# Kernel tuning notes

Measured on AMD Instinct MI355X. Metric: run time of the kernel, lower is better.

## Reference

```python
import jax, jax.numpy as jnp
import numpy as np
import math

B, S, D, H = 2, 2048, 1024, 16
HD = D // H  # 64


def _rope(x, cos, sin):
    # x: [B,S,H,HD]; cos/sin: [S, HD//2]
    x2 = x.reshape(*x.shape[:-1], HD // 2, 2)
    x0, x1 = x2[..., 0], x2[..., 1]
    c = cos[None, :, None, :]
    s = sin[None, :, None, :]
    r0 = x0 * c - x1 * s
    r1 = x0 * s + x1 * c
    return jnp.stack([r0, r1], axis=-1).reshape(x.shape)


def setup_inputs() -> dict:
    key = jax.random.key(0)
    ks = jax.random.split(key, 6)
    x = jax.random.normal(ks[0], (B, S, D), dtype=jnp.float32)
    wq = jax.random.normal(ks[1], (D, D), dtype=jnp.float32) * 0.02
    wk = jax.random.normal(ks[2], (D, D), dtype=jnp.float32) * 0.02
    wv = jax.random.normal(ks[3], (D, D), dtype=jnp.float32) * 0.02
    wo = jax.random.normal(ks[4], (D, D), dtype=jnp.float32) * 0.02
    # standard RoPE frequencies: theta = 10000^(-2i/HD)
    inv_freq = 1.0 / (10000.0 ** (jnp.arange(0, HD, 2, dtype=jnp.float32) / HD))
    t = jnp.arange(S, dtype=jnp.float32)
    ang = t[:, None] * inv_freq[None, :]  # [S, HD//2]
    freqs_cos = jnp.cos(ang)
    freqs_sin = jnp.sin(ang)
    # causal additive mask [S, S]
    mask = jnp.where(jnp.tril(jnp.ones((S, S), dtype=bool)), 0.0, -1e9).astype(jnp.float32)
    return {"x": x, "wq": wq, "wk": wk, "wv": wv, "wo": wo,
            "freqs_cos": freqs_cos, "freqs_sin": freqs_sin, "mask": mask}


def reference(x, wq, wk, wv, wo, freqs_cos, freqs_sin, mask):
    b, s, d = x.shape
    # nn.Linear with no bias: y = x @ W^T
    q = jnp.einsum('bsd,od->bso', x, wq).reshape(b, s, H, HD)
    k = jnp.einsum('bsd,od->bso', x, wk).reshape(b, s, H, HD)
    v = jnp.einsum('bsd,od->bso', x, wv).reshape(b, s, H, HD)
    q = _rope(q, freqs_cos, freqs_sin)
    k = _rope(k, freqs_cos, freqs_sin)
    # [B,H,S,HD]
    q = q.transpose(0, 2, 1, 3)
    k = k.transpose(0, 2, 1, 3)
    v = v.transpose(0, 2, 1, 3)
    scores = jnp.einsum('bhqd,bhkd->bhqk', q, k) / math.sqrt(HD)
    scores = scores + mask[None, None, :, :]
    p = jax.nn.softmax(scores.astype(jnp.float32), axis=-1).astype(q.dtype)
    out = jnp.einsum('bhqk,bhkd->bhqd', p, v)
    out = out.transpose(0, 2, 1, 3).reshape(b, s, d)
    return jnp.einsum('bsd,od->bso', out, wo)
```

## Files before the change

### kernel.cpp

```cpp
#include <hip/hip_runtime.h>
#include <hip/hip_bf16.h>
#include <stdint.h>

#define NB 2
#define NS 2048
#define ND 1024
#define NH 16
#define NM (NB*NS)

typedef __attribute__((ext_vector_type(8))) short bf16x8;
typedef __attribute__((ext_vector_type(4))) float f32x4;

static __device__ __forceinline__ f32x4 mfma16(bf16x8 a, bf16x8 b, f32x4 c) {
  return __builtin_amdgcn_mfma_f32_16x16x32_bf16(a, b, c, 0, 0, 0);
}

static __device__ __forceinline__ void gload_lds16(const void* g, void* l) {
  __builtin_amdgcn_global_load_lds(
      (const __attribute__((address_space(1))) void*)g,
      (__attribute__((address_space(3))) void*)l, 16, 0, 0);
}

static __device__ __forceinline__ uint32_t pkbf2(float a, float b) {
  return (uint32_t)__bfloat16_as_ushort(__float2bfloat16(a)) |
         ((uint32_t)__bfloat16_as_ushort(__float2bfloat16(b)) << 16);
}

#define QSCALE 0.18033688011112042f

struct alignas(8) bh4 { __hip_bfloat16 x, y, z, w; };

__global__ void cvt_bf16(const float* __restrict__ in,
                         __hip_bfloat16* __restrict__ out, int n4) {
  int i = blockIdx.x * blockDim.x + threadIdx.x;
  int stride = gridDim.x * blockDim.x;
  for (; i < n4; i += stride) {
    float4 v = reinterpret_cast<const float4*>(in)[i];
    bh4 o;
    o.x = __float2bfloat16(v.x);
    o.y = __float2bfloat16(v.y);
    o.z = __float2bfloat16(v.z);
    o.w = __float2bfloat16(v.w);
    reinterpret_cast<bh4*>(out)[i] = o;
  }
}

__global__ void cvt_w4(const float* __restrict__ w0, const float* __restrict__ w1,
                       const float* __restrict__ w2, const float* __restrict__ w3,
                       __hip_bfloat16* o0, __hip_bfloat16* o1,
                       __hip_bfloat16* o2, __hip_bfloat16* o3) {
  const int t = blockIdx.x >> 10;
  const float* in = (t == 0) ? w0 : (t == 1) ? w1 : (t == 2) ? w2 : w3;
  __hip_bfloat16* out = (t == 0) ? o0 : (t == 1) ? o1 : (t == 2) ? o2 : o3;
  const int i = (blockIdx.x & 1023) * 256 + threadIdx.x;
  float4 v = reinterpret_cast<const float4*>(in)[i];
  bh4 o;
  o.x = __float2bfloat16(v.x);
  o.y = __float2bfloat16(v.y);
  o.z = __float2bfloat16(v.z);
  o.w = __float2bfloat16(v.w);
  reinterpret_cast<bh4*>(out)[i] = o;
}

__global__ __launch_bounds__(256) void gemm_qkv(
    const __hip_bfloat16* __restrict__ A,
    const __hip_bfloat16* __restrict__ Wq,
    const __hip_bfloat16* __restrict__ Wk,
    const __hip_bfloat16* __restrict__ Wv,
    const float* __restrict__ fcos,
    const float* __restrict__ fsin,
    __hip_bfloat16* __restrict__ Qo,
    __hip_bfloat16* __restrict__ Ko,
    __hip_bfloat16* __restrict__ Vo) {
  __shared__ __hip_bfloat16 sA[128 * 32];
  __shared__ __hip_bfloat16 sB[128 * 32];

  const int wsel = blockIdx.y >> 3;
  const __hip_bfloat16* W = (wsel == 0) ? Wq : (wsel == 1) ? Wk : Wv;

  const int tid = threadIdx.x;
  const int wid = tid >> 6;
  const int lane = tid & 63;
  const int l4 = lane >> 4, l16 = lane & 15;
  const int brow = blockIdx.x * 128;
  const int bcol = (blockIdx.y & 7) * 128;
  const int wr = (wid >> 1) * 64;
  const int wc = (wid & 1) * 64;

  f32x4 acc[4][4] = {};

  const __hip_bfloat16* Ap = A + (size_t)(brow + (tid >> 2)) * 1024 + (tid & 3) * 8;
  const __hip_bfloat16* Wp = W + (size_t)(bcol + (tid >> 2)) * 1024 + (tid & 3) * 8;
  char* sAc = (char*)sA + wid * 1024;
  char* sBc = (char*)sB + wid * 1024;

  for (int kt = 0; kt < 32; ++kt) {
    const int k0 = kt * 32;
    __syncthreads();
    gload_lds16(Ap + k0,             sAc);
    gload_lds16(Ap + 64 * 1024 + k0, sAc + 4096);
    gload_lds16(Wp + k0,             sBc);
    gload_lds16(Wp + 64 * 1024 + k0, sBc + 4096);
    __syncthreads();

    bf16x8 af[4], bfr[4];
#pragma unroll
    for (int i = 0; i < 4; ++i)
      af[i] = *(const bf16x8*)&sA[(wr + i * 16 + l16) * 32 + l4 * 8];
#pragma unroll
    for (int i = 0; i < 4; ++i)
      bfr[i] = *(const bf16x8*)&sB[(wc + i * 16 + l16) * 32 + l4 * 8];
#pragma unroll
    for (int mi = 0; mi < 4; ++mi)
#pragma unroll
      for (int ni = 0; ni < 4; ++ni)
        acc[mi][ni] = mfma16(af[mi], bfr[ni], acc[mi][ni]);
  }

#pragma unroll
  for (int mi = 0; mi < 4; ++mi)
#pragma unroll
    for (int ni = 0; ni < 4; ++ni)
#pragma unroll
      for (int j = 0; j < 4; ++j) {
        float v = acc[mi][ni][j];
        const int row = brow + wr + mi * 16 + l4 * 4 + j;
        const int col = bcol + wc + ni * 16 + l16;
        const int bb = row >> 11, ss = row & 2047;
        const int hh = col >> 6, hd = col & 63;
        if (wsel == 2) {
          Vo[((size_t)(bb * 16 + hh) * 64 + hd) * 2048 + ss] = __float2bfloat16(v);
        } else {
          float other = __shfl_xor(v, 1);
          const int p = hd >> 1;
          const float c = fcos[ss * 32 + p];
          const float sn = fsin[ss * 32 + p];
          float r = (col & 1) ? (other * sn + v * c) : (v * c - other * sn);
          __hip_bfloat16* dst = (wsel == 0) ? Qo : Ko;
          if (wsel == 0) r *= QSCALE;
          dst[((size_t)(bb * 16 + hh) * 2048 + ss) * 64 + hd] = __float2bfloat16(r);
        }
      }
}

__global__ __launch_bounds__(256) void gemm_out(
    const __hip_bfloat16* __restrict__ A,
    const __hip_bfloat16* __restrict__ W,
    float* __restrict__ C) {
  __shared__ __hip_bfloat16 sA[64 * 32];
  __shared__ __hip_bfloat16 sB[128 * 32];

  const int tid = threadIdx.x;
  const int wid = tid >> 6;
  const int lane = tid & 63;
  const int l4 = lane >> 4, l16 = lane & 15;
  const int brow = blockIdx.x * 64;
  const int bcol = blockIdx.y * 128;
  const int wr = (wid & 1) * 32;
  const int wc = (wid >> 1) * 64;

  f32x4 acc[2][4] = {};

  const __hip_bfloat16* Ap = A + (size_t)(brow + (tid >> 2)) * 1024 + (tid & 3) * 8;
  const __hip_bfloat16* Wp = W + (size_t)(bcol + (tid >> 2)) * 1024 + (tid & 3) * 8;
  char* sAc = (char*)sA + wid * 1024;
  char* sBc = (char*)sB + wid * 1024;

  for (int kt = 0; kt < 32; ++kt) {
    const int k0 = kt * 32;
    __syncthreads();
    gload_lds16(Ap + k0,             sAc);
    gload_lds16(Wp + k0,             sBc);
    gload_lds16(Wp + 64 * 1024 + k0, sBc + 4096);
    __syncthreads();

    bf16x8 af[2], bfr[4];
#pragma unroll
    for (int i = 0; i < 2; ++i)
      af[i] = *(const bf16x8*)&sA[(wr + i * 16 + l16) * 32 + l4 * 8];
#pragma unroll
    for (int i = 0; i < 4; ++i)
      bfr[i] = *(const bf16x8*)&sB[(wc + i * 16 + l16) * 32 + l4 * 8];
#pragma unroll
    for (int mi = 0; mi < 2; ++mi)
#pragma unroll
      for (int ni = 0; ni < 4; ++ni)
        acc[mi][ni] = mfma16(af[mi], bfr[ni], acc[mi][ni]);
  }

#pragma unroll
  for (int mi = 0; mi < 2; ++mi)
#pragma unroll
    for (int ni = 0; ni < 4; ++ni)
#pragma unroll
      for (int j = 0; j < 4; ++j) {
        const int row = brow + wr + mi * 16 + l4 * 4 + j;
        const int col = bcol + wc + ni * 16 + l16;
        C[(size_t)row * 1024 + col] = acc[mi][ni][j];
      }
}

__global__ __launch_bounds__(64) void attn_fwd(
    const __hip_bfloat16* __restrict__ Q,
    const __hip_bfloat16* __restrict__ K,
    const __hip_bfloat16* __restrict__ VT,
    __hip_bfloat16* __restrict__ AO) {
  const int L = blockIdx.x;
  const int g = 63 - (L >> 5);
  const int bh = L & 31;
  const int bb = bh >> 4;
  const int hh = bh & 15;
  const int lane = threadIdx.x & 63;
  const int l4 = lane >> 4, l16 = lane & 15;
  const int wq0 = g * 32;

  const __hip_bfloat16* Qg = Q + (size_t)bh * 2048 * 64;
  const __hip_bfloat16* Kg = K + (size_t)bh * 2048 * 64;
  const __hip_bfloat16* Vg = VT + (size_t)bh * 64 * 2048;

  __shared__ __hip_bfloat16 sP[32][72];

  bf16x8 qf[2][2];
#pragma unroll
  for (int q2 = 0; q2 < 2; ++q2)
#pragma unroll
    for (int dk = 0; dk < 2; ++dk)
      qf[q2][dk] = *(const bf16x8*)&Qg[(size_t)(wq0 + q2 * 16 + l16) * 64 + dk * 32 + l4 * 8];

  float mrun[2] = {-1e30f, -1e30f};
  float lrun[2] = {0.f, 0.f};
  f32x4 oacc[2][4] = {};

  const int lastkv = (wq0 + 31) >> 6;
  for (int kv = 0; kv <= lastkv; ++kv) {
    const int kb = kv * 64;

    bf16x8 kfr[4][2];
#pragma unroll
    for (int kf = 0; kf < 4; ++kf)
#pragma unroll
      for (int dk = 0; dk < 2; ++dk)
        kfr[kf][dk] = *(const bf16x8*)&Kg[(size_t)(kb + kf * 16 + l16) * 64 + dk * 32 + l4 * 8];

    f32x4 sacc[4][2] = {};
    __builtin_amdgcn_s_setprio(1);
#pragma unroll
    for (int dk = 0; dk < 2; ++dk)
#pragma unroll
      for (int kf = 0; kf < 4; ++kf)
#pragma unroll
        for (int q2 = 0; q2 < 2; ++q2)
          sacc[kf][q2] = mfma16(kfr[kf][dk], qf[q2][dk], sacc[kf][q2]);
    __builtin_amdgcn_s_setprio(0);

    bf16x8 vfr[4][2];
#pragma unroll
    for (int df = 0; df < 4; ++df)
#pragma unroll
      for (int ks = 0; ks < 2; ++ks)
        vfr[df][ks] = *(const bf16x8*)&Vg[(size_t)(df * 16 + l16) * 2048 + kb + ks * 32 + l4 * 8];

    const bool need_mask = (kb + 63 > wq0);
    float fac[2];
#pragma unroll
    for (int q2 = 0; q2 < 2; ++q2) {
      const int qi = wq0 + q2 * 16 + l16;
      float pv[16];
#pragma unroll
      for (int kf = 0; kf < 4; ++kf)
#pragma unroll
        for (int j = 0; j < 4; ++j) {
          float s = sacc[kf][q2][j];
          if (need_mask && (kb + kf * 16 + l4 * 4 + j > qi)) s = -1e30f;
          pv[kf * 4 + j] = s;
        }
      float m0 = fmaxf(fmaxf(pv[0], pv[1]), fmaxf(pv[2], pv[3]));
      float m1 = fmaxf(fmaxf(pv[4], pv[5]), fmaxf(pv[6], pv[7]));
      float m2 = fmaxf(fmaxf(pv[8], pv[9]), fmaxf(pv[10], pv[11]));
      float m3 = fmaxf(fmaxf(pv[12], pv[13]), fmaxf(pv[14], pv[15]));
      float mloc = fmaxf(fmaxf(m0, m1), fmaxf(m2, m3));
      mloc = fmaxf(mloc, __shfl_xor(mloc, 16));
      mloc = fmaxf(mloc, __shfl_xor(mloc, 32));
      const float mold = mrun[q2];
      const float mnew = fmaxf(mold, mloc);
      const float f = exp2f(mold - mnew);
      fac[q2] = f;
      mrun[q2] = mnew;
      float ts = 0.f;
      float pe[16];
#pragma unroll
      for (int t = 0; t < 16; ++t) { pe[t] = exp2f(pv[t] - mnew); ts += pe[t]; }
#pragma unroll
      for (int kf = 0; kf < 4; ++kf) {
        uint2 w;
        w.x = pkbf2(pe[kf * 4 + 0], pe[kf * 4 + 1]);
        w.y = pkbf2(pe[kf * 4 + 2], pe[kf * 4 + 3]);
        *(uint2*)&sP[q2 * 16 + l16][kf * 16 + l4 * 4] = w;
      }
      ts += __shfl_xor(ts, 16);
      ts += __shfl_xor(ts, 32);
      lrun[q2] = lrun[q2] * f + ts;
    }

#pragma unroll
    for (int mf = 0; mf < 2; ++mf)
#pragma unroll
      for (int j = 0; j < 4; ++j) {
        const float fr = __shfl(fac[mf], l4 * 4 + j);
#pragma unroll
        for (int df = 0; df < 4; ++df) oacc[mf][df][j] *= fr;
      }

    __builtin_amdgcn_s_setprio(1);
#pragma unroll
    for (int ks = 0; ks < 2; ++ks) {
      bf16x8 pfr[2];
#pragma unroll
      for (int mf = 0; mf < 2; ++mf)
        pfr[mf] = *(const bf16x8*)&sP[mf * 16 + l16][ks * 32 + l4 * 8];
#pragma unroll
      for (int mf = 0; mf < 2; ++mf)
#pragma unroll
        for (int df = 0; df < 4; ++df)
          oacc[mf][df] = mfma16(pfr[mf], vfr[df][ks], oacc[mf][df]);
    }
    __builtin_amdgcn_s_setprio(0);
  }

  float inv[2];
#pragma unroll
  for (int q2 = 0; q2 < 2; ++q2) inv[q2] = 1.f / lrun[q2];
#pragma unroll
  for (int mf = 0; mf < 2; ++mf)
#pragma unroll
    for (int j = 0; j < 4; ++j) {
      const float ir = __shfl(inv[mf], l4 * 4 + j);
      const int ss = wq0 + mf * 16 + l4 * 4 + j;
#pragma unroll
      for (int df = 0; df < 4; ++df) {
        const int dd = hh * 64 + df * 16 + l16;
        AO[((size_t)bb * 2048 + ss) * 1024 + dd] =
            __float2bfloat16(oacc[mf][df][j] * ir);
      }
    }
}

extern "C" void kernel_launch(void* const* d_in, const int* in_sizes, int n_in,
                              void* d_out, int out_size, void* d_ws, size_t ws_size,
                              hipStream_t stream) {
  const float* x  = (const float*)d_in[0];
  const float* wq = (const float*)d_in[1];
  const float* wk = (const float*)d_in[2];
  const float* wv = (const float*)d_in[3];
  const float* wo = (const float*)d_in[4];
  const float* fc = (const float*)d_in[5];
  const float* fs = (const float*)d_in[6];

  char* ws = (char*)d_ws;
  const size_t MB = 1024 * 1024;
  __hip_bfloat16* xb  = (__hip_bfloat16*)(ws);
  __hip_bfloat16* wqb = (__hip_bfloat16*)(ws + 8 * MB);
  __hip_bfloat16* wkb = (__hip_bfloat16*)(ws + 10 * MB);
  __hip_bfloat16* wvb = (__hip_bfloat16*)(ws + 12 * MB);
  __hip_bfloat16* wob = (__hip_bfloat16*)(ws + 14 * MB);
  __hip_bfloat16* qws = (__hip_bfloat16*)(ws + 16 * MB);
  __hip_bfloat16* kws = (__hip_bfloat16*)(ws + 24 * MB);
  __hip_bfloat16* vws = (__hip_bfloat16*)(ws + 32 * MB);
  __hip_bfloat16* ao  = (__hip_bfloat16*)(ws + 40 * MB);

  cvt_bf16<<<2048, 256, 0, stream>>>(x, xb, NM * ND / 4);
  cvt_w4<<<4096, 256, 0, stream>>>(wq, wk, wv, wo, wqb, wkb, wvb, wob);

  gemm_qkv<<<dim3(NM / 128, 24), 256, 0, stream>>>(xb, wqb, wkb, wvb, fc, fs,
                                                   qws, kws, vws);

  attn_fwd<<<dim3(2048), 64, 0, stream>>>(qws, kws, vws, ao);

  gemm_out<<<dim3(NM / 64, ND / 128), 256, 0, stream>>>(ao, wob, (float*)d_out);
}
```

Baseline: 244.9 us.

## Merge conversion kernels, stage RoPE/V transpose in LDS, widen attention blocks with K prefetch

Replaces the two fp32-to-bf16 conversion launches with a single combined kernel. The QKV GEMM epilogue now caches cos/sin tables in shared memory and transposes the V tile through LDS, so V is written with coalesced 16-byte stores instead of scattered 2-byte ones. Attention blocks now hold four waves covering 128 queries each, with a reordered block schedule that pairs heavy and light causal tiles, and K fragments are double-buffered so the next tile's load is issued ahead. The extra LDS (about 33 KB) lowers GEMM occupancy, and the larger attention blocks reduce scheduling granularity.

```diff
diff --git a/kernel.cpp b/kernel.cpp
--- a/kernel.cpp
+++ b/kernel.cpp
@@ -30,29 +30,22 @@
 
 struct alignas(8) bh4 { __hip_bfloat16 x, y, z, w; };
 
-__global__ void cvt_bf16(const float* __restrict__ in,
-                         __hip_bfloat16* __restrict__ out, int n4) {
-  int i = blockIdx.x * blockDim.x + threadIdx.x;
-  int stride = gridDim.x * blockDim.x;
-  for (; i < n4; i += stride) {
-    float4 v = reinterpret_cast<const float4*>(in)[i];
-    bh4 o;
-    o.x = __float2bfloat16(v.x);
-    o.y = __float2bfloat16(v.y);
-    o.z = __float2bfloat16(v.z);
-    o.w = __float2bfloat16(v.w);
-    reinterpret_cast<bh4*>(out)[i] = o;
-  }
-}
-
-__global__ void cvt_w4(const float* __restrict__ w0, const float* __restrict__ w1,
-                       const float* __restrict__ w2, const float* __restrict__ w3,
-                       __hip_bfloat16* o0, __hip_bfloat16* o1,
-                       __hip_bfloat16* o2, __hip_bfloat16* o3) {
-  const int t = blockIdx.x >> 10;
-  const float* in = (t == 0) ? w0 : (t == 1) ? w1 : (t == 2) ? w2 : w3;
-  __hip_bfloat16* out = (t == 0) ? o0 : (t == 1) ? o1 : (t == 2) ? o2 : o3;
-  const int i = (blockIdx.x & 1023) * 256 + threadIdx.x;
+__global__ void cvt_all(const float* __restrict__ x,
+                        const float* __restrict__ w0, const float* __restrict__ w1,
+                        const float* __restrict__ w2, const float* __restrict__ w3,
+                        __hip_bfloat16* xb, __hip_bfloat16* o0, __hip_bfloat16* o1,
+                        __hip_bfloat16* o2, __hip_bfloat16* o3) {
+  const int b = blockIdx.x;
+  const float* in;
+  __hip_bfloat16* out;
+  int i;
+  if (b < 4096) { in = x; out = xb; i = b * 256 + threadIdx.x; }
+  else {
+    const int t = (b - 4096) >> 10;
+    in  = (t == 0) ? w0 : (t == 1) ? w1 : (t == 2) ? w2 : w3;
+    out = (t == 0) ? o0 : (t == 1) ? o1 : (t == 2) ? o2 : o3;
+    i = ((b - 4096) & 1023) * 256 + threadIdx.x;
+  }
   float4 v = reinterpret_cast<const float4*>(in)[i];
   bh4 o;
   o.x = __float2bfloat16(v.x);
@@ -74,6 +67,7 @@
     __hip_bfloat16* __restrict__ Vo) {
   __shared__ __hip_bfloat16 sA[128 * 32];
   __shared__ __hip_bfloat16 sB[128 * 32];
+  __shared__ __align__(16) char xtr[33792];
 
   const int wsel = blockIdx.y >> 3;
   const __hip_bfloat16* W = (wsel == 0) ? Wq : (wsel == 1) ? Wk : Wv;
@@ -86,6 +80,23 @@
   const int bcol = (blockIdx.y & 7) * 128;
   const int wr = (wid >> 1) * 64;
   const int wc = (wid & 1) * 64;
+  const int ss0 = brow & 2047;
+  const int bbb = brow >> 11;
+
+  if (wsel < 2) {
+    float2* tab = (float2*)xtr;
+#pragma unroll
+    for (int i = 0; i < 4; ++i) {
+      const int e = i * 1024 + tid * 4;
+      const int ssl = e >> 5, p = e & 31;
+      float4 c4 = *(const float4*)&fcos[(ss0 + ssl) * 32 + p];
+      float4 s4 = *(const float4*)&fsin[(ss0 + ssl) * 32 + p];
+      tab[ssl * 33 + p + 0] = {c4.x, s4.x};
+      tab[ssl * 33 + p + 1] = {c4.y, s4.y};
+      tab[ssl * 33 + p + 2] = {c4.z, s4.z};
+      tab[ssl * 33 + p + 3] = {c4.w, s4.w};
+    }
+  }
 
   f32x4 acc[4][4] = {};
 
@@ -117,30 +128,57 @@
         acc[mi][ni] = mfma16(af[mi], bfr[ni], acc[mi][ni]);
   }
 
-#pragma unroll
-  for (int mi = 0; mi < 4; ++mi)
-#pragma unroll
-    for (int ni = 0; ni < 4; ++ni)
-#pragma unroll
-      for (int j = 0; j < 4; ++j) {
-        float v = acc[mi][ni][j];
-        const int row = brow + wr + mi * 16 + l4 * 4 + j;
-        const int col = bcol + wc + ni * 16 + l16;
-        const int bb = row >> 11, ss = row & 2047;
-        const int hh = col >> 6, hd = col & 63;
-        if (wsel == 2) {
-          Vo[((size_t)(bb * 16 + hh) * 64 + hd) * 2048 + ss] = __float2bfloat16(v);
-        } else {
+  if (wsel == 2) {
+    __hip_bfloat16 (*tt)[132] = (__hip_bfloat16(*)[132])xtr;
+#pragma unroll
+    for (int h = 0; h < 2; ++h) {
+      __syncthreads();
+      if ((wid & 1) == h) {
+#pragma unroll
+        for (int mi = 0; mi < 4; ++mi)
+#pragma unroll
+          for (int ni = 0; ni < 4; ++ni) {
+            const int c = ni * 16 + l16;
+            const int r0 = wr + mi * 16 + l4 * 4;
+            uint2 w;
+            w.x = pkbf2(acc[mi][ni][0], acc[mi][ni][1]);
+            w.y = pkbf2(acc[mi][ni][2], acc[mi][ni][3]);
+            *(uint2*)&tt[c][r0] = w;
+          }
+      }
+      __syncthreads();
+      const int cl = tid >> 2;
+      const int rq = (tid & 3) * 32;
+      const int o = bcol + h * 64 + cl;
+      const int hh = o >> 6, hd = o & 63;
+      __hip_bfloat16* dst =
+          Vo + ((size_t)(bbb * 16 + hh) * 64 + hd) * 2048 + ss0 + rq;
+#pragma unroll
+      for (int k2 = 0; k2 < 4; ++k2)
+        *(uint4*)&dst[k2 * 8] = *(const uint4*)&tt[cl][rq + k2 * 8];
+    }
+  } else {
+    const float2* tab = (const float2*)xtr;
+    __hip_bfloat16* dst = (wsel == 0) ? Qo : Ko;
+#pragma unroll
+    for (int mi = 0; mi < 4; ++mi)
+#pragma unroll
+      for (int ni = 0; ni < 4; ++ni)
+#pragma unroll
+        for (int j = 0; j < 4; ++j) {
+          float v = acc[mi][ni][j];
+          const int rloc = wr + mi * 16 + l4 * 4 + j;
+          const int col = bcol + wc + ni * 16 + l16;
+          const int hh = col >> 6, hd = col & 63;
           float other = __shfl_xor(v, 1);
-          const int p = hd >> 1;
-          const float c = fcos[ss * 32 + p];
-          const float sn = fsin[ss * 32 + p];
-          float r = (col & 1) ? (other * sn + v * c) : (v * c - other * sn);
-          __hip_bfloat16* dst = (wsel == 0) ? Qo : Ko;
+          const float2 cs = tab[rloc * 33 + (hd >> 1)];
+          float r = (col & 1) ? (other * cs.y + v * cs.x)
+                              : (v * cs.x - other * cs.y);
           if (wsel == 0) r *= QSCALE;
-          dst[((size_t)(bb * 16 + hh) * 2048 + ss) * 64 + hd] = __float2bfloat16(r);
+          dst[((size_t)(bbb * 16 + hh) * 2048 + ss0 + rloc) * 64 + hd] =
+              __float2bfloat16(r);
         }
-      }
+  }
 }
 
 __global__ __launch_bounds__(256) void gemm_out(
@@ -200,25 +238,28 @@
       }
 }
 
-__global__ __launch_bounds__(64) void attn_fwd(
+__global__ __launch_bounds__(256) void attn_fwd(
     const __hip_bfloat16* __restrict__ Q,
     const __hip_bfloat16* __restrict__ K,
     const __hip_bfloat16* __restrict__ VT,
     __hip_bfloat16* __restrict__ AO) {
   const int L = blockIdx.x;
-  const int g = 63 - (L >> 5);
-  const int bh = L & 31;
+  int qt, bh;
+  if (L < 256) { qt = 15 - (L >> 5); bh = L & 31; }
+  else         { qt = (L >> 5) - 8;  bh = L & 31; }
   const int bb = bh >> 4;
   const int hh = bh & 15;
-  const int lane = threadIdx.x & 63;
+  const int tid = threadIdx.x;
+  const int wid = tid >> 6;
+  const int lane = tid & 63;
   const int l4 = lane >> 4, l16 = lane & 15;
-  const int wq0 = g * 32;
+  const int wq0 = qt * 128 + wid * 32;
 
   const __hip_bfloat16* Qg = Q + (size_t)bh * 2048 * 64;
   const __hip_bfloat16* Kg = K + (size_t)bh * 2048 * 64;
   const __hip_bfloat16* Vg = VT + (size_t)bh * 64 * 2048;
 
-  __shared__ __hip_bfloat16 sP[32][72];
+  __shared__ __hip_bfloat16 sP[4][32][72];
 
   bf16x8 qf[2][2];
 #pragma unroll
@@ -232,15 +273,25 @@
   f32x4 oacc[2][4] = {};
 
   const int lastkv = (wq0 + 31) >> 6;
-  for (int kv = 0; kv <= lastkv; ++kv) {
+
+  bf16x8 kA[4][2], kB[4][2];
+#pragma unroll
+  for (int kf = 0; kf < 4; ++kf)
+#pragma unroll
+    for (int dk = 0; dk < 2; ++dk)
+      kA[kf][dk] = *(const bf16x8*)&Kg[(size_t)(kf * 16 + l16) * 64 + dk * 32 + l4 * 8];
+
+  auto step = [&](int kv, bf16x8 (&kc)[4][2], bf16x8 (&kn)[4][2]) {
     const int kb = kv * 64;
 
-    bf16x8 kfr[4][2];
-#pragma unroll
-    for (int kf = 0; kf < 4; ++kf)
-#pragma unroll
-      for (int dk = 0; dk < 2; ++dk)
-        kfr[kf][dk] = *(const bf16x8*)&Kg[(size_t)(kb + kf * 16 + l16) * 64 + dk * 32 + l4 * 8];
+    if (kv + 1 <= lastkv) {
+      const int kb2 = kb + 64;
+#pragma unroll
+      for (int kf = 0; kf < 4; ++kf)
+#pragma unroll
+        for (int dk = 0; dk < 2; ++dk)
+          kn[kf][dk] = *(const bf16x8*)&Kg[(size_t)(kb2 + kf * 16 + l16) * 64 + dk * 32 + l4 * 8];
+    }
 
     f32x4 sacc[4][2] = {};
     __builtin_amdgcn_s_setprio(1);
@@ -250,7 +301,7 @@
       for (int kf = 0; kf < 4; ++kf)
 #pragma unroll
         for (int q2 = 0; q2 < 2; ++q2)
-          sacc[kf][q2] = mfma16(kfr[kf][dk], qf[q2][dk], sacc[kf][q2]);
+          sacc[kf][q2] = mfma16(kc[kf][dk], qf[q2][dk], sacc[kf][q2]);
     __builtin_amdgcn_s_setprio(0);
 
     bf16x8 vfr[4][2];
@@ -295,7 +346,7 @@
         uint2 w;
         w.x = pkbf2(pe[kf * 4 + 0], pe[kf * 4 + 1]);
         w.y = pkbf2(pe[kf * 4 + 2], pe[kf * 4 + 3]);
-        *(uint2*)&sP[q2 * 16 + l16][kf * 16 + l4 * 4] = w;
+        *(uint2*)&sP[wid][q2 * 16 + l16][kf * 16 + l4 * 4] = w;
       }
       ts += __shfl_xor(ts, 16);
       ts += __shfl_xor(ts, 32);
@@ -317,7 +368,7 @@
       bf16x8 pfr[2];
 #pragma unroll
       for (int mf = 0; mf < 2; ++mf)
-        pfr[mf] = *(const bf16x8*)&sP[mf * 16 + l16][ks * 32 + l4 * 8];
+        pfr[mf] = *(const bf16x8*)&sP[wid][mf * 16 + l16][ks * 32 + l4 * 8];
 #pragma unroll
       for (int mf = 0; mf < 2; ++mf)
 #pragma unroll
@@ -325,6 +376,12 @@
           oacc[mf][df] = mfma16(pfr[mf], vfr[df][ks], oacc[mf][df]);
     }
     __builtin_amdgcn_s_setprio(0);
+  };
+
+  for (int kv = 0; kv <= lastkv; kv += 2) {
+    step(kv, kA, kB);
+    if (kv + 1 > lastkv) break;
+    step(kv + 1, kB, kA);
   }
 
   float inv[2];
@@ -368,13 +425,12 @@
   __hip_bfloat16* vws = (__hip_bfloat16*)(ws + 32 * MB);
   __hip_bfloat16* ao  = (__hip_bfloat16*)(ws + 40 * MB);
 
-  cvt_bf16<<<2048, 256, 0, stream>>>(x, xb, NM * ND / 4);
-  cvt_w4<<<4096, 256, 0, stream>>>(wq, wk, wv, wo, wqb, wkb, wvb, wob);
+  cvt_all<<<8192, 256, 0, stream>>>(x, wq, wk, wv, wo, xb, wqb, wkb, wvb, wob);
 
   gemm_qkv<<<dim3(NM / 128, 24), 256, 0, stream>>>(xb, wqb, wkb, wvb, fc, fs,
                                                    qws, kws, vws);
 
-  attn_fwd<<<dim3(2048), 64, 0, stream>>>(qws, kws, vws, ao);
+  attn_fwd<<<dim3(512), 256, 0, stream>>>(qws, kws, vws, ao);
 
   gemm_out<<<dim3(NM / 64, ND / 128), 256, 0, stream>>>(ao, wob, (float*)d_out);
 }
```

Result: slower. 255.8 us (+4.5%).
